# Kernel optimization log

Measured on AMD Instinct MI355X. Metric: run time of the kernel, lower is better.

The kernel has to match this reference:

```python
import jax, jax.numpy as jnp
import numpy as np

N_IN, D_IN, N_OUT, D_OUT = 1152, 8, 10, 16
ROUTINGS, NUM_BG = 3, 1
C, H, W = 1, 28, 28
BATCH = 128
DEC_IN = N_OUT * D_OUT  # 160, projection_type=None -> dec_feature_size = outcaps_size


def squash(x, axis=-1):
    norm = jnp.linalg.norm(x, axis=axis, keepdims=True)
    scale = norm ** 2 / (1.0 + norm ** 2) / (norm + 1e-8)
    return scale * x


def scale_coef(x, num_bg):
    # x: [B, n_out] or [B, n_out, n_in]; min/max normalize over dim 1,
    # excluding the last num_bg (background) capsules, then floor at 0.5.
    if num_bg > 0:
        xm = x[:, : x.shape[1] - num_bg]
    else:
        xm = x
    mn = jnp.min(xm, axis=1, keepdims=True)
    mx = jnp.max(xm, axis=1, keepdims=True)
    out = (xm - mn) / jnp.maximum(mx - mn, 1e-6)  # vrange (0,1)
    if num_bg > 0:
        out = jnp.concatenate([out, jnp.zeros_like(out[:, :num_bg])], axis=1)
    return jnp.maximum(out, 0.5)


def decode(capsflat, W1, b1, W2, b2, W3, b3):
    # fcn decoder (eval mode: dropout is identity): 160 -> 512 -> 1024 -> C*H*W
    h = jax.nn.relu(capsflat @ W1 + b1)
    h = jax.nn.relu(h @ W2 + b2)
    return jax.nn.sigmoid(h @ W3 + b3)


def setup_inputs() -> dict:
    key = jax.random.key(0)
    ks = jax.random.split(key, 9)
    return {
        'incaps': jax.random.normal(ks[0], (BATCH, N_IN, D_IN), jnp.float32),
        'x_input': jax.random.uniform(ks[1], (BATCH, C, H, W), jnp.float32),
        'weight': 0.1 * jax.random.normal(ks[2], (N_OUT, N_IN, D_OUT, D_IN), jnp.float32),
        'W1': 0.05 * jax.random.normal(ks[3], (DEC_IN, 512), jnp.float32),
        'b1': jnp.zeros((512,), jnp.float32),
        'W2': 0.05 * jax.random.normal(ks[4], (512, 1024), jnp.float32),
        'b2': jnp.zeros((1024,), jnp.float32),
        'W3': 0.05 * jax.random.normal(ks[5], (1024, C * H * W), jnp.float32),
        'b3': jnp.zeros((C * H * W,), jnp.float32),
    }


def reference(incaps, x_input, weight, W1, b1, W2, b2, W3, b3):
    B = incaps.shape[0]
    # outcaps_hat: matmul(weight, incaps[:,None,:,:,None]).squeeze(-1)
    hat = jnp.einsum('nkoi,bki->bnko', weight, incaps)  # [B, n_out, n_in, d_out]
    hat_d = jax.lax.stop_gradient(hat)
    rc = jnp.ones((B, N_OUT, N_IN), hat.dtype)
    eye = jnp.eye(N_OUT, dtype=hat.dtype)
    x_flat = x_input.reshape(B, 1, -1)
    for _ in range(ROUTINGS - 1):
        # squash over capsule dim, weighted sum over input capsules
        outcaps = squash(jnp.sum(rc[..., None] * hat_d, axis=2, keepdims=True))  # [B,n,1,d]
        b = jnp.sum(outcaps * hat_d, axis=-1)  # agreement [B, n_out, n_in]
        c = scale_coef(b, NUM_BG)
        objcaps = outcaps[:, :, 0, :]  # [B, n_out, d_out]
        # get_every_obj_rscore vectorized: mask one object capsule at a time
        masked = objcaps[:, None, :, :] * eye[None, :, :, None]  # [B, n_obj, n_out, d]
        recon = decode(masked.reshape(B, N_OUT, DEC_IN), W1, b1, W2, b2, W3, b3)  # [B,n_obj,CHW]
        rscore = -jnp.sum((x_flat - recon) ** 2, axis=-1)  # neg MSE-sum, [B, n_obj]
        r = scale_coef(rscore, NUM_BG)
        rc = c * r[:, :, None]
    # final iteration uses non-detached hat
    outcaps = squash(jnp.sum(rc[..., None] * hat, axis=2, keepdims=True))
    return outcaps[:, :, 0, :]  # [B, n_out, d_out]
```

## Files before the change

kernel.cpp:

```cpp
#include <hip/hip_runtime.h>
#include <math.h>

#define BATCH  128
#define NIN    1152
#define DIN    8
#define NOUTC  10
#define DOUT   16
#define H1DIM  512
#define H2DIM  1024
#define PIX    784
#define NROWS  (BATCH * NOUTC)
#define NBY3   13

typedef __attribute__((ext_vector_type(8))) __bf16 bf16x8;
typedef __attribute__((ext_vector_type(4))) float  f32x4;
typedef __attribute__((ext_vector_type(4))) unsigned int u32x4;

__device__ __forceinline__ float bf2f(unsigned int u) {
    union { unsigned int i; float f; } v; v.i = u << 16; return v.f;
}
__device__ __forceinline__ ushort f2bf(float f) {
    union { float f; unsigned int i; } v; v.f = f;
    unsigned int r = v.i + 0x7FFFu + ((v.i >> 16) & 1u);
    return (ushort)(r >> 16);
}
__device__ __forceinline__ float ldin(const void* p, size_t i, int isbf) {
    return isbf ? bf2f(((const ushort*)p)[i]) : ((const float*)p)[i];
}
__device__ __forceinline__ bf16x8 ld_frag(const ushort* p) {
    uint4 u = *(const uint4*)p;
    return __builtin_bit_cast(bf16x8, u);
}
__device__ __forceinline__ float dot8(uint4 a, uint4 b) {
    float s;
    s  = bf2f(a.x & 0xffffu) * bf2f(b.x & 0xffffu);
    s += bf2f(a.x >> 16)     * bf2f(b.x >> 16);
    s += bf2f(a.y & 0xffffu) * bf2f(b.y & 0xffffu);
    s += bf2f(a.y >> 16)     * bf2f(b.y >> 16);
    s += bf2f(a.z & 0xffffu) * bf2f(b.z & 0xffffu);
    s += bf2f(a.z >> 16)     * bf2f(b.z >> 16);
    s += bf2f(a.w & 0xffffu) * bf2f(b.w & 0xffffu);
    s += bf2f(a.w >> 16)     * bf2f(b.w >> 16);
    return s;
}

struct PrepArgs {
    const void* src[9];
    ushort*     dst[9];
    int         n[9];
    int*        flag;
};

__global__ __launch_bounds__(256) void prep_kernel(PrepArgs a)
{
    __shared__ int cntS;
    __shared__ ushort tile[32][33];
    int tid = threadIdx.x;
    if (tid == 0) cntS = 0;
    __syncthreads();
    {
        const ushort* wu = (const ushort*)a.src[0];
        int c = 0;
        for (int s = tid; s < 512; s += 256) {
            int e = (wu[s * 2] >> 7) & 0xFF;
            if (e >= 88 && e <= 140) c++;
        }
        atomicAdd(&cntS, c);
    }
    __syncthreads();
    int isbf = (cntS >= 384) ? 1 : 0;
    int seg = blockIdx.y;
    if (seg == 0 && blockIdx.x == 0 && tid == 0) *a.flag = isbf;

    if (seg <= 6) {
        int n = a.n[seg];
        int stride = gridDim.x * 256;
        ushort* d = a.dst[seg];
        if (isbf) {
            const ushort* s = (const ushort*)a.src[seg];
            for (int i = blockIdx.x * 256 + tid; i < n; i += stride) d[i] = s[i];
        } else {
            const float* s = (const float*)a.src[seg];
            for (int i = blockIdx.x * 256 + tid; i < n; i += stride) d[i] = f2bf(s[i]);
        }
        return;
    }
    int R = (seg == 7) ? H1DIM : H2DIM;
    int C = (seg == 7) ? H2DIM : PIX;
    int tilesX = (seg == 7) ? 32 : 25;
    int tilesY = (seg == 7) ? 16 : 32;
    int t = blockIdx.x;
    if (t >= tilesX * tilesY) return;
    int tx2 = t % tilesX, ty2 = t / tilesX;
    int c0 = tx2 * 32, r0 = ty2 * 32;
    const void* in = a.src[seg];
    ushort* out = a.dst[seg];
    int tx = tid & 31, ty = tid >> 5;
    for (int i = ty; i < 32; i += 8) {
        int r = r0 + i, c = c0 + tx;
        tile[i][tx] = (r < R && c < C) ? f2bf(ldin(in, (size_t)r * C + c, isbf)) : (ushort)0;
    }
    __syncthreads();
    for (int i = ty; i < 32; i += 8) {
        int c = c0 + i, r = r0 + tx;
        if (c < C && r < R) out[(size_t)c * R + r] = tile[tx][i];
    }
}

__global__ __launch_bounds__(256) void hat_build(
    const ushort* __restrict__ icvt,
    const ushort* __restrict__ wcvt,
    ushort* __restrict__ hatG)
{
    int kc = blockIdx.x, bc = blockIdx.y, n = blockIdx.z;
    int t  = threadIdx.x;
    int k  = kc * 128 + (t >> 1);
    int oh = (t & 1) << 3;

    const uint4* wp = (const uint4*)(wcvt + (((size_t)n * NIN + k) * DOUT + oh) * DIN);
    uint4 wr[8];
    #pragma unroll
    for (int j = 0; j < 8; j++) wr[j] = wp[j];

    int b0 = bc * 16;
    #pragma unroll 4
    for (int bl = 0; bl < 16; bl++) {
        int b = b0 + bl;
        uint4 iu = *(const uint4*)(icvt + ((size_t)b * NIN + k) * DIN);
        unsigned int h[8];
        #pragma unroll
        for (int j = 0; j < 8; j++) h[j] = f2bf(dot8(wr[j], iu));
        u32x4 ov = { h[0] | (h[1] << 16), h[2] | (h[3] << 16),
                     h[4] | (h[5] << 16), h[6] | (h[7] << 16) };
        __builtin_nontemporal_store(ov,
            (u32x4*)(hatG + (((size_t)(b * NOUTC + n) * NIN + k) * DOUT + oh)));
    }
}

template<bool COMPUTE>
__global__ __launch_bounds__(512, 8) void reduce_pass(
    const ushort* __restrict__ hatG,
    const ushort* __restrict__ icvt,
    const ushort* __restrict__ wcvt,
    const ushort* __restrict__ bsPrev,
    const float*  __restrict__ partials,
    int iter0,
    const ushort* __restrict__ W1c,
    const ushort* __restrict__ b1c,
    ushort* __restrict__ h1out,
    ushort* __restrict__ bsOut,
    void*   __restrict__ outFinal,
    const int* __restrict__ flagp)
{
    int bn  = blockIdx.x;
    int n   = bn % NOUTC;
    int b   = bn / NOUTC;
    int tid = threadIdx.x;

    __shared__ uint4  hatS4[NIN * DOUT / 8];
    __shared__ ushort wSb[NIN];
    __shared__ float  redS[8][16];
    __shared__ float  sumS[16];
    __shared__ float  ocS[16];
    __shared__ float  scaleS;
    ushort* hatS = (ushort*)hatS4;

    if constexpr (COMPUTE) {
        __shared__ uint4 incS4[NIN * DIN / 8];
        const uint4* incp = (const uint4*)(icvt + (size_t)b * NIN * DIN);
        for (int i = tid; i < NIN * DIN / 8; i += 512) incS4[i] = incp[i];
        __syncthreads();
        const ushort* incS = (const ushort*)incS4;
        const ushort* wp = wcvt + (size_t)n * NIN * DOUT * DIN;
        for (int idx = tid; idx < NIN * DOUT; idx += 512) {
            int k = idx >> 4;
            uint4 wu = *(const uint4*)(wp + (size_t)idx * 8);
            uint4 iu = *(const uint4*)(incS + k * 8);
            hatS[idx] = f2bf(dot8(wu, iu));
        }
    } else {
        const u32x4* hp = (const u32x4*)(hatG + (size_t)bn * NIN * DOUT);
        for (int i = tid; i < NIN * DOUT / 8; i += 512) {
            u32x4 v = __builtin_nontemporal_load(hp + i);
            hatS4[i] = __builtin_bit_cast(uint4, v);
        }
    }

    if (!iter0) {
        if (tid < 9) {
            float s = 0.f;
            #pragma unroll
            for (int j = 0; j < NBY3; j++)
                s += partials[(size_t)(b * NOUTC + tid) * 16 + j];
            sumS[tid] = -s;
        }
        __syncthreads();
        float mn = 1e30f, mx = -1e30f;
        #pragma unroll
        for (int n2 = 0; n2 < 9; n2++) {
            float v = sumS[n2];
            mn = fminf(mn, v); mx = fmaxf(mx, v);
        }
        float den = fmaxf(mx - mn, 1e-6f);
        float rv = (n < 9) ? fmaxf((sumS[n] - mn) / den, 0.5f) : 0.5f;
        for (int k = tid; k < NIN; k += 512) {
            float c = 0.5f;
            if (n < 9) {
                float vv[9], mn2 = 1e30f, mx2 = -1e30f;
                #pragma unroll
                for (int n2 = 0; n2 < 9; n2++) {
                    vv[n2] = bf2f(bsPrev[(size_t)(b * NOUTC + n2) * NIN + k]);
                    mn2 = fminf(mn2, vv[n2]); mx2 = fmaxf(mx2, vv[n2]);
                }
                float den2 = fmaxf(mx2 - mn2, 1e-6f);
                c = fmaxf((vv[n] - mn2) / den2, 0.5f);
            }
            wSb[k] = f2bf(c * rv);
        }
    }
    __syncthreads();

    int h = tid & 1, kb = tid >> 1;
    int wave = tid >> 6, lane = tid & 63;
    float acc[8];
    #pragma unroll
    for (int o = 0; o < 8; o++) acc[o] = 0.f;
    #pragma unroll
    for (int j = 0; j < 4; j++) {
        int k = kb + 256 * j;
        float w = iter0 ? 1.f : bf2f(wSb[k]);
        bf16x8 hv = ld_frag(hatS + k * 16 + h * 8);
        #pragma unroll
        for (int o = 0; o < 8; o++) acc[o] += w * (float)hv[o];
    }
    if (kb < 128) {
        int k = 1024 + kb;
        float w = iter0 ? 1.f : bf2f(wSb[k]);
        bf16x8 hv = ld_frag(hatS + k * 16 + h * 8);
        #pragma unroll
        for (int o = 0; o < 8; o++) acc[o] += w * (float)hv[o];
    }
    #pragma unroll
    for (int off = 32; off >= 2; off >>= 1) {
        #pragma unroll
        for (int o = 0; o < 8; o++) acc[o] += __shfl_xor(acc[o], off);
    }
    if (lane < 2) {
        #pragma unroll
        for (int o = 0; o < 8; o++) redS[wave][lane * 8 + o] = acc[o];
    }
    __syncthreads();
    if (tid < 16) {
        float s = 0.f;
        #pragma unroll
        for (int wv = 0; wv < 8; wv++) s += redS[wv][tid];
        sumS[tid] = s;
    }
    __syncthreads();
    if (tid == 0) {
        float n2 = 0.f;
        #pragma unroll
        for (int o = 0; o < 16; o++) n2 += sumS[o] * sumS[o];
        float nrm = sqrtf(n2);
        scaleS = n2 / (1.f + n2) / (nrm + 1e-8f);
    }
    __syncthreads();
    if (tid < 16) {
        float oc = scaleS * sumS[tid];
        ocS[tid] = oc;
        if (outFinal) {
            if (*flagp) ((ushort*)outFinal)[(size_t)bn * 16 + tid] = f2bf(oc);
            else        ((float*) outFinal)[(size_t)bn * 16 + tid] = oc;
        }
    }
    __syncthreads();

    if (bsOut) {
        #pragma unroll
        for (int j = 0; j < 4; j++) {
            int k = kb + 256 * j;
            bf16x8 hv = ld_frag(hatS + k * 16 + h * 8);
            float s = 0.f;
            #pragma unroll
            for (int o = 0; o < 8; o++) s += ocS[h * 8 + o] * (float)hv[o];
            s += __shfl_xor(s, 1);
            if (h == 0) bsOut[(size_t)bn * NIN + k] = f2bf(s);
        }
        if (kb < 128) {
            int k = 1024 + kb;
            bf16x8 hv = ld_frag(hatS + k * 16 + h * 8);
            float s = 0.f;
            #pragma unroll
            for (int o = 0; o < 8; o++) s += ocS[h * 8 + o] * (float)hv[o];
            s += __shfl_xor(s, 1);
            if (h == 0) bsOut[(size_t)bn * NIN + k] = f2bf(s);
        }
    }

    if (h1out) {
        int col = tid;
        float acc1 = bf2f(b1c[col]);
        #pragma unroll
        for (int i = 0; i < 16; i++)
            acc1 += ocS[i] * bf2f(W1c[(size_t)(n * 16 + i) * H1DIM + col]);
        h1out[(size_t)bn * H1DIM + col] = f2bf(fmaxf(acc1, 0.f));
    }
}

__global__ __launch_bounds__(256) void gemm_kernel(
    const ushort* __restrict__ A, const ushort* __restrict__ Bt,
    const ushort* __restrict__ bias, int K, int N,
    ushort* __restrict__ Cout,
    const ushort* __restrict__ xin, float* __restrict__ partials)
{
    int m0 = blockIdx.x * 64, n0 = blockIdx.y * 64;
    int tid = threadIdx.x;
    int wave = tid >> 6, lane = tid & 63, quad = lane >> 4, l16 = lane & 15;

    __shared__ uint4 As4[320];
    __shared__ uint4 Bs4[320];
    ushort* As = (ushort*)As4;
    ushort* Bs = (ushort*)Bs4;

    f32x4 acc[4];
    #pragma unroll
    for (int nt = 0; nt < 4; nt++)
        #pragma unroll
        for (int rg = 0; rg < 4; rg++) acc[nt][rg] = 0.f;

    int sMi = tid >> 2, sKk = (tid & 3) * 8;
    int sLds = sMi * 5 + (tid & 3);
    const ushort* Ap = A + (size_t)(m0 + sMi) * K + sKk;
    const ushort* Bp = Bt + (size_t)(n0 + sMi) * K + sKk;
    bool bOK = (n0 + sMi) < N;

    uint4 aR = *(const uint4*)Ap;
    uint4 bR = bOK ? *(const uint4*)Bp : make_uint4(0, 0, 0, 0);

    for (int k0 = 0; k0 < K; k0 += 32) {
        As4[sLds] = aR;
        Bs4[sLds] = bR;
        __syncthreads();
        if (k0 + 32 < K) {
            aR = *(const uint4*)(Ap + k0 + 32);
            bR = bOK ? *(const uint4*)(Bp + k0 + 32) : make_uint4(0, 0, 0, 0);
        }
        bf16x8 a = ld_frag(As + (wave * 16 + l16) * 40 + quad * 8);
        #pragma unroll
        for (int nt = 0; nt < 4; nt++) {
            bf16x8 bb = ld_frag(Bs + (nt * 16 + l16) * 40 + quad * 8);
            acc[nt] = __builtin_amdgcn_mfma_f32_16x16x32_bf16(a, bb, acc[nt], 0, 0, 0);
        }
        __syncthreads();
    }

    int rowBase = m0 + wave * 16 + quad * 4;
    if (Cout) {
        #pragma unroll
        for (int nt = 0; nt < 4; nt++) {
            int col = n0 + nt * 16 + l16;
            float bv = bf2f(bias[col]);
            #pragma unroll
            for (int rg = 0; rg < 4; rg++) {
                float v = acc[nt][rg] + bv;
                Cout[(size_t)(rowBase + rg) * N + col] = f2bf(fmaxf(v, 0.f));
            }
        }
    } else {
        float vr[4] = {0.f, 0.f, 0.f, 0.f};
        #pragma unroll
        for (int nt = 0; nt < 4; nt++) {
            int col = n0 + nt * 16 + l16;
            if (col < N) {
                float bv = bf2f(bias[col]);
                #pragma unroll
                for (int rg = 0; rg < 4; rg++) {
                    int row = rowBase + rg;
                    int bb = row / NOUTC;
                    float z = acc[nt][rg] + bv;
                    float s = 1.f / (1.f + __expf(-z));
                    float d = bf2f(xin[(size_t)bb * PIX + col]) - s;
                    vr[rg] += d * d;
                }
            }
        }
        #pragma unroll
        for (int rg = 0; rg < 4; rg++) {
            float v = vr[rg];
            #pragma unroll
            for (int off = 8; off >= 1; off >>= 1) v += __shfl_xor(v, off, 16);
            if (l16 == 0)
                partials[(size_t)(rowBase + rg) * 16 + blockIdx.y] = v;
        }
    }
}

extern "C" void kernel_launch(void* const* d_in, const int* in_sizes, int n_in,
                              void* d_out, int out_size, void* d_ws, size_t ws_size,
                              hipStream_t stream)
{
    const void* inc = d_in[0];
    const void* x   = d_in[1];
    const void* w   = d_in[2];
    const void* W1  = d_in[3];
    const void* b1  = d_in[4];
    const void* W2  = d_in[5];
    const void* b2  = d_in[6];
    const void* W3  = d_in[7];
    const void* b3  = d_in[8];

    char* p = (char*)d_ws;
    auto alloc = [&](size_t bytes) { void* r = p; p += (bytes + 255) & ~(size_t)255; return r; };
    int*    flagWS    = (int*)alloc(256);
    ushort* bsA       = (ushort*)alloc((size_t)NROWS * NIN * 2);
    ushort* bsB       = (ushort*)alloc((size_t)NROWS * NIN * 2);
    float*  partials  = (float*)alloc((size_t)NROWS * 16 * 4);
    ushort* h1WS      = (ushort*)alloc((size_t)NROWS * H1DIM * 2);
    ushort* h2WS      = (ushort*)alloc((size_t)NROWS * H2DIM * 2);
    ushort* W2T       = (ushort*)alloc((size_t)H2DIM * H1DIM * 2);
    ushort* W3T       = (ushort*)alloc((size_t)PIX * H2DIM * 2);
    ushort* wcvt      = (ushort*)alloc((size_t)NOUTC * NIN * DOUT * DIN * 2);
    ushort* icvt      = (ushort*)alloc((size_t)BATCH * NIN * DIN * 2);
    ushort* W1c       = (ushort*)alloc((size_t)160 * H1DIM * 2);
    ushort* b1c       = (ushort*)alloc((size_t)H1DIM * 2);
    ushort* b2c       = (ushort*)alloc((size_t)H2DIM * 2);
    ushort* b3c       = (ushort*)alloc((size_t)PIX * 2);
    ushort* xc        = (ushort*)alloc((size_t)BATCH * PIX * 2);
    ushort* hatG      = (ushort*)alloc((size_t)NROWS * NIN * DOUT * 2);
    bool haveHat = ((char*)hatG + (size_t)NROWS * NIN * DOUT * 2) <= ((char*)d_ws + ws_size);

    PrepArgs pa;
    pa.src[0] = w;   pa.dst[0] = wcvt; pa.n[0] = NOUTC * NIN * DOUT * DIN;
    pa.src[1] = inc; pa.dst[1] = icvt; pa.n[1] = BATCH * NIN * DIN;
    pa.src[2] = W1;  pa.dst[2] = W1c;  pa.n[2] = 160 * H1DIM;
    pa.src[3] = b1;  pa.dst[3] = b1c;  pa.n[3] = H1DIM;
    pa.src[4] = b2;  pa.dst[4] = b2c;  pa.n[4] = H2DIM;
    pa.src[5] = b3;  pa.dst[5] = b3c;  pa.n[5] = PIX;
    pa.src[6] = x;   pa.dst[6] = xc;   pa.n[6] = BATCH * PIX;
    pa.src[7] = W2;  pa.dst[7] = W2T;  pa.n[7] = 0;
    pa.src[8] = W3;  pa.dst[8] = W3T;  pa.n[8] = 0;
    pa.flag = flagWS;
    prep_kernel<<<dim3(800, 9), 256, 0, stream>>>(pa);

    if (haveHat) hat_build<<<dim3(9, 8, NOUTC), 256, 0, stream>>>(icvt, wcvt, hatG);

    if (haveHat)
        reduce_pass<false><<<NROWS, 512, 0, stream>>>(
            hatG, icvt, wcvt, nullptr, nullptr, 1,
            W1c, b1c, h1WS, bsA, nullptr, flagWS);
    else
        reduce_pass<true><<<NROWS, 512, 0, stream>>>(
            nullptr, icvt, wcvt, nullptr, nullptr, 1,
            W1c, b1c, h1WS, bsA, nullptr, flagWS);

    for (int it = 0; it < 2; it++) {
        gemm_kernel<<<dim3(NROWS / 64, H2DIM / 64), 256, 0, stream>>>(
            h1WS, W2T, b2c, H1DIM, H2DIM, h2WS, nullptr, nullptr);
        gemm_kernel<<<dim3(NROWS / 64, NBY3), 256, 0, stream>>>(
            h2WS, W3T, b3c, H2DIM, PIX, nullptr, xc, partials);

        int last = (it == 1);
        const ushort* bsP = (it == 0) ? bsA : bsB;
        ushort* bsO       = last ? nullptr : bsB;
        ushort* h1o       = last ? nullptr : h1WS;
        void*   fin       = last ? d_out : nullptr;
        if (haveHat)
            reduce_pass<false><<<NROWS, 512, 0, stream>>>(
                hatG, icvt, wcvt, bsP, partials, 0,
                W1c, b1c, h1o, bsO, fin, flagWS);
        else
            reduce_pass<true><<<NROWS, 512, 0, stream>>>(
                nullptr, icvt, wcvt, bsP, partials, 0,
                W1c, b1c, h1o, bsO, fin, flagWS);
    }
}
```

Baseline: 215.3 us.

## Read raw inputs in hat_build and keep hat fragments in registers in reduce_pass

Drops the separate bf16 conversion of the capsule weight and input tensors from the prep kernel. hat_build and the compute fallback now read the raw inputs directly and convert them on the fly, after detecting the input dtype. In the main reduce_pass path, each thread keeps its hat fragments in registers instead of staging the whole 36 KB hat tile through shared memory, and only the tail rows go to shared memory. This cuts the LDS footprint and shared-memory traffic, and the occupancy hint is lowered to 4 to make room for the extra register pressure.

```diff
diff --git a/kernel.cpp b/kernel.cpp
--- a/kernel.cpp
+++ b/kernel.cpp
@@ -27,9 +27,11 @@
 __device__ __forceinline__ float ldin(const void* p, size_t i, int isbf) {
     return isbf ? bf2f(((const ushort*)p)[i]) : ((const float*)p)[i];
 }
+__device__ __forceinline__ bf16x8 frag_of(uint4 u) {
+    return __builtin_bit_cast(bf16x8, u);
+}
 __device__ __forceinline__ bf16x8 ld_frag(const ushort* p) {
-    uint4 u = *(const uint4*)p;
-    return __builtin_bit_cast(bf16x8, u);
+    return frag_of(*(const uint4*)p);
 }
 __device__ __forceinline__ float dot8(uint4 a, uint4 b) {
     float s;
@@ -43,11 +45,35 @@
     s += bf2f(a.w >> 16)     * bf2f(b.w >> 16);
     return s;
 }
+__device__ __forceinline__ uint4 pack8(float4 a, float4 b) {
+    uint4 r;
+    r.x = f2bf(a.x) | ((unsigned)f2bf(a.y) << 16);
+    r.y = f2bf(a.z) | ((unsigned)f2bf(a.w) << 16);
+    r.z = f2bf(b.x) | ((unsigned)f2bf(b.y) << 16);
+    r.w = f2bf(b.z) | ((unsigned)f2bf(b.w) << 16);
+    return r;
+}
+
+__device__ __forceinline__ int detect_bf(const void* w, int* cntS) {
+    int tid = threadIdx.x, nt = blockDim.x;
+    if (tid == 0) *cntS = 0;
+    __syncthreads();
+    const ushort* u = (const ushort*)w;
+    int c = 0;
+    for (int s = tid; s < 512; s += nt) {
+        int e = (u[s * 2] >> 7) & 0xFF;
+        if (e >= 88 && e <= 140) c++;
+    }
+    atomicAdd(cntS, c);
+    __syncthreads();
+    return (*cntS >= 384) ? 1 : 0;
+}
 
 struct PrepArgs {
-    const void* src[9];
-    ushort*     dst[9];
-    int         n[9];
+    const void* w;
+    const void* src[7];
+    ushort*     dst[7];
+    int         n[7];
     int*        flag;
 };
 
@@ -56,23 +82,11 @@
     __shared__ int cntS;
     __shared__ ushort tile[32][33];
     int tid = threadIdx.x;
-    if (tid == 0) cntS = 0;
-    __syncthreads();
-    {
-        const ushort* wu = (const ushort*)a.src[0];
-        int c = 0;
-        for (int s = tid; s < 512; s += 256) {
-            int e = (wu[s * 2] >> 7) & 0xFF;
-            if (e >= 88 && e <= 140) c++;
-        }
-        atomicAdd(&cntS, c);
-    }
-    __syncthreads();
-    int isbf = (cntS >= 384) ? 1 : 0;
+    int isbf = detect_bf(a.w, &cntS);
     int seg = blockIdx.y;
     if (seg == 0 && blockIdx.x == 0 && tid == 0) *a.flag = isbf;
 
-    if (seg <= 6) {
+    if (seg <= 4) {
         int n = a.n[seg];
         int stride = gridDim.x * 256;
         ushort* d = a.dst[seg];
@@ -85,10 +99,10 @@
         }
         return;
     }
-    int R = (seg == 7) ? H1DIM : H2DIM;
-    int C = (seg == 7) ? H2DIM : PIX;
-    int tilesX = (seg == 7) ? 32 : 25;
-    int tilesY = (seg == 7) ? 16 : 32;
+    int R = (seg == 5) ? H1DIM : H2DIM;
+    int C = (seg == 5) ? H2DIM : PIX;
+    int tilesX = (seg == 5) ? 32 : 25;
+    int tilesY = (seg == 5) ? 16 : 32;
     int t = blockIdx.x;
     if (t >= tilesX * tilesY) return;
     int tx2 = t % tilesX, ty2 = t / tilesX;
@@ -108,25 +122,40 @@
 }
 
 __global__ __launch_bounds__(256) void hat_build(
-    const ushort* __restrict__ icvt,
-    const ushort* __restrict__ wcvt,
+    const void* __restrict__ inc,
+    const void* __restrict__ w,
     ushort* __restrict__ hatG)
 {
+    __shared__ int cntS;
+    int isbf = detect_bf(w, &cntS);
     int kc = blockIdx.x, bc = blockIdx.y, n = blockIdx.z;
     int t  = threadIdx.x;
     int k  = kc * 128 + (t >> 1);
     int oh = (t & 1) << 3;
 
-    const uint4* wp = (const uint4*)(wcvt + (((size_t)n * NIN + k) * DOUT + oh) * DIN);
+    size_t wbase = ((size_t)n * NIN + k) * DOUT + oh;
     uint4 wr[8];
-    #pragma unroll
-    for (int j = 0; j < 8; j++) wr[j] = wp[j];
+    if (isbf) {
+        const uint4* wp = (const uint4*)((const ushort*)w + wbase * DIN);
+        #pragma unroll
+        for (int j = 0; j < 8; j++) wr[j] = wp[j];
+    } else {
+        const float4* wp = (const float4*)((const float*)w + wbase * DIN);
+        #pragma unroll
+        for (int j = 0; j < 8; j++) wr[j] = pack8(wp[2 * j], wp[2 * j + 1]);
+    }
 
     int b0 = bc * 16;
     #pragma unroll 4
     for (int bl = 0; bl < 16; bl++) {
         int b = b0 + bl;
-        uint4 iu = *(const uint4*)(icvt + ((size_t)b * NIN + k) * DIN);
+        size_t ioff = ((size_t)b * NIN + k) * DIN;
+        uint4 iu;
+        if (isbf) iu = *(const uint4*)((const ushort*)inc + ioff);
+        else {
+            const float4* ip = (const float4*)((const float*)inc + ioff);
+            iu = pack8(ip[0], ip[1]);
+        }
         unsigned int h[8];
         #pragma unroll
         for (int j = 0; j < 8; j++) h[j] = f2bf(dot8(wr[j], iu));
@@ -138,10 +167,10 @@
 }
 
 template<bool COMPUTE>
-__global__ __launch_bounds__(512, 8) void reduce_pass(
+__global__ __launch_bounds__(512, 4) void reduce_pass(
     const ushort* __restrict__ hatG,
-    const ushort* __restrict__ icvt,
-    const ushort* __restrict__ wcvt,
+    const void*   __restrict__ incRaw,
+    const void*   __restrict__ wRaw,
     const ushort* __restrict__ bsPrev,
     const float*  __restrict__ partials,
     int iter0,
@@ -157,33 +186,47 @@
     int b   = bn / NOUTC;
     int tid = threadIdx.x;
 
-    __shared__ uint4  hatS4[NIN * DOUT / 8];
     __shared__ ushort wSb[NIN];
     __shared__ float  redS[8][16];
     __shared__ float  sumS[16];
     __shared__ float  ocS[16];
     __shared__ float  scaleS;
-    ushort* hatS = (ushort*)hatS4;
-
-    if constexpr (COMPUTE) {
-        __shared__ uint4 incS4[NIN * DIN / 8];
-        const uint4* incp = (const uint4*)(icvt + (size_t)b * NIN * DIN);
-        for (int i = tid; i < NIN * DIN / 8; i += 512) incS4[i] = incp[i];
-        __syncthreads();
-        const ushort* incS = (const ushort*)incS4;
-        const ushort* wp = wcvt + (size_t)n * NIN * DOUT * DIN;
+
+    int h = tid & 1, kb = tid >> 1;
+    int wave = tid >> 6, lane = tid & 63;
+
+    uint4 v[4];
+    const ushort* tailS;
+
+    if constexpr (!COMPUTE) {
+        __shared__ uint4 hatTail4[256];
+        const ushort* hbase = hatG + (size_t)bn * NIN * DOUT;
+        #pragma unroll
+        for (int j = 0; j < 4; j++)
+            v[j] = *(const uint4*)(hbase + ((kb + 256 * j) * DOUT + h * 8));
+        if (tid < 256)
+            hatTail4[tid] = *(const uint4*)(hbase + 1024 * DOUT + tid * 8);
+        tailS = (const ushort*)hatTail4;
+    } else {
+        __shared__ int cntS;
+        __shared__ uint4 hatS4[NIN * DOUT / 8];
+        int isbf = detect_bf(wRaw, &cntS);
+        size_t wnb = (size_t)n * NIN * DOUT * DIN;
         for (int idx = tid; idx < NIN * DOUT; idx += 512) {
             int k = idx >> 4;
-            uint4 wu = *(const uint4*)(wp + (size_t)idx * 8);
-            uint4 iu = *(const uint4*)(incS + k * 8);
-            hatS[idx] = f2bf(dot8(wu, iu));
-        }
-    } else {
-        const u32x4* hp = (const u32x4*)(hatG + (size_t)bn * NIN * DOUT);
-        for (int i = tid; i < NIN * DOUT / 8; i += 512) {
-            u32x4 v = __builtin_nontemporal_load(hp + i);
-            hatS4[i] = __builtin_bit_cast(uint4, v);
-        }
+            float s = 0.f;
+            #pragma unroll
+            for (int i = 0; i < 8; i++)
+                s += ldin(wRaw, wnb + (size_t)idx * 8 + i, isbf) *
+                     ldin(incRaw, ((size_t)b * NIN + k) * DIN + i, isbf);
+            ((ushort*)hatS4)[idx] = f2bf(s);
+        }
+        __syncthreads();
+        const ushort* hbase = (const ushort*)hatS4;
+        #pragma unroll
+        for (int j = 0; j < 4; j++)
+            v[j] = *(const uint4*)(hbase + ((kb + 256 * j) * DOUT + h * 8));
+        tailS = hbase + 1024 * DOUT;
     }
 
     if (!iter0) {
@@ -198,8 +241,8 @@
         float mn = 1e30f, mx = -1e30f;
         #pragma unroll
         for (int n2 = 0; n2 < 9; n2++) {
-            float v = sumS[n2];
-            mn = fminf(mn, v); mx = fmaxf(mx, v);
+            float vv = sumS[n2];
+            mn = fminf(mn, vv); mx = fmaxf(mx, vv);
         }
         float den = fmaxf(mx - mn, 1e-6f);
         float rv = (n < 9) ? fmaxf((sumS[n] - mn) / den, 0.5f) : 0.5f;
@@ -220,8 +263,6 @@
     }
     __syncthreads();
 
-    int h = tid & 1, kb = tid >> 1;
-    int wave = tid >> 6, lane = tid & 63;
     float acc[8];
     #pragma unroll
     for (int o = 0; o < 8; o++) acc[o] = 0.f;
@@ -229,14 +270,14 @@
     for (int j = 0; j < 4; j++) {
         int k = kb + 256 * j;
         float w = iter0 ? 1.f : bf2f(wSb[k]);
-        bf16x8 hv = ld_frag(hatS + k * 16 + h * 8);
+        bf16x8 hv = frag_of(v[j]);
         #pragma unroll
         for (int o = 0; o < 8; o++) acc[o] += w * (float)hv[o];
     }
-    if (kb < 128) {
+    if (tid < 256) {
         int k = 1024 + kb;
         float w = iter0 ? 1.f : bf2f(wSb[k]);
-        bf16x8 hv = ld_frag(hatS + k * 16 + h * 8);
+        bf16x8 hv = ld_frag(tailS + kb * DOUT + h * 8);
         #pragma unroll
         for (int o = 0; o < 8; o++) acc[o] += w * (float)hv[o];
     }
@@ -276,24 +317,25 @@
     __syncthreads();
 
     if (bsOut) {
+        float o0 = ocS[h * 8 + 0], o1 = ocS[h * 8 + 1], o2 = ocS[h * 8 + 2],
+              o3 = ocS[h * 8 + 3], o4 = ocS[h * 8 + 4], o5 = ocS[h * 8 + 5],
+              o6 = ocS[h * 8 + 6], o7 = ocS[h * 8 + 7];
         #pragma unroll
         for (int j = 0; j < 4; j++) {
-            int k = kb + 256 * j;
-            bf16x8 hv = ld_frag(hatS + k * 16 + h * 8);
-            float s = 0.f;
-            #pragma unroll
-            for (int o = 0; o < 8; o++) s += ocS[h * 8 + o] * (float)hv[o];
+            bf16x8 hv = frag_of(v[j]);
+            float s = o0 * (float)hv[0] + o1 * (float)hv[1] + o2 * (float)hv[2] +
+                      o3 * (float)hv[3] + o4 * (float)hv[4] + o5 * (float)hv[5] +
+                      o6 * (float)hv[6] + o7 * (float)hv[7];
             s += __shfl_xor(s, 1);
-            if (h == 0) bsOut[(size_t)bn * NIN + k] = f2bf(s);
-        }
-        if (kb < 128) {
-            int k = 1024 + kb;
-            bf16x8 hv = ld_frag(hatS + k * 16 + h * 8);
-            float s = 0.f;
-            #pragma unroll
-            for (int o = 0; o < 8; o++) s += ocS[h * 8 + o] * (float)hv[o];
+            if (h == 0) bsOut[(size_t)bn * NIN + kb + 256 * j] = f2bf(s);
+        }
+        if (tid < 256) {
+            bf16x8 hv = ld_frag(tailS + kb * DOUT + h * 8);
+            float s = o0 * (float)hv[0] + o1 * (float)hv[1] + o2 * (float)hv[2] +
+                      o3 * (float)hv[3] + o4 * (float)hv[4] + o5 * (float)hv[5] +
+                      o6 * (float)hv[6] + o7 * (float)hv[7];
             s += __shfl_xor(s, 1);
-            if (h == 0) bsOut[(size_t)bn * NIN + k] = f2bf(s);
+            if (h == 0) bsOut[(size_t)bn * NIN + 1024 + kb] = f2bf(s);
         }
     }
 
@@ -419,8 +461,6 @@
     ushort* h2WS      = (ushort*)alloc((size_t)NROWS * H2DIM * 2);
     ushort* W2T       = (ushort*)alloc((size_t)H2DIM * H1DIM * 2);
     ushort* W3T       = (ushort*)alloc((size_t)PIX * H2DIM * 2);
-    ushort* wcvt      = (ushort*)alloc((size_t)NOUTC * NIN * DOUT * DIN * 2);
-    ushort* icvt      = (ushort*)alloc((size_t)BATCH * NIN * DIN * 2);
     ushort* W1c       = (ushort*)alloc((size_t)160 * H1DIM * 2);
     ushort* b1c       = (ushort*)alloc((size_t)H1DIM * 2);
     ushort* b2c       = (ushort*)alloc((size_t)H2DIM * 2);
@@ -430,27 +470,26 @@
     bool haveHat = ((char*)hatG + (size_t)NROWS * NIN * DOUT * 2) <= ((char*)d_ws + ws_size);
 
     PrepArgs pa;
-    pa.src[0] = w;   pa.dst[0] = wcvt; pa.n[0] = NOUTC * NIN * DOUT * DIN;
-    pa.src[1] = inc; pa.dst[1] = icvt; pa.n[1] = BATCH * NIN * DIN;
-    pa.src[2] = W1;  pa.dst[2] = W1c;  pa.n[2] = 160 * H1DIM;
-    pa.src[3] = b1;  pa.dst[3] = b1c;  pa.n[3] = H1DIM;
-    pa.src[4] = b2;  pa.dst[4] = b2c;  pa.n[4] = H2DIM;
-    pa.src[5] = b3;  pa.dst[5] = b3c;  pa.n[5] = PIX;
-    pa.src[6] = x;   pa.dst[6] = xc;   pa.n[6] = BATCH * PIX;
-    pa.src[7] = W2;  pa.dst[7] = W2T;  pa.n[7] = 0;
-    pa.src[8] = W3;  pa.dst[8] = W3T;  pa.n[8] = 0;
+    pa.w = w;
+    pa.src[0] = W1;  pa.dst[0] = W1c;  pa.n[0] = 160 * H1DIM;
+    pa.src[1] = b1;  pa.dst[1] = b1c;  pa.n[1] = H1DIM;
+    pa.src[2] = b2;  pa.dst[2] = b2c;  pa.n[2] = H2DIM;
+    pa.src[3] = b3;  pa.dst[3] = b3c;  pa.n[3] = PIX;
+    pa.src[4] = x;   pa.dst[4] = xc;   pa.n[4] = BATCH * PIX;
+    pa.src[5] = W2;  pa.dst[5] = W2T;  pa.n[5] = 0;
+    pa.src[6] = W3;  pa.dst[6] = W3T;  pa.n[6] = 0;
     pa.flag = flagWS;
-    prep_kernel<<<dim3(800, 9), 256, 0, stream>>>(pa);
-
-    if (haveHat) hat_build<<<dim3(9, 8, NOUTC), 256, 0, stream>>>(icvt, wcvt, hatG);
+    prep_kernel<<<dim3(800, 7), 256, 0, stream>>>(pa);
+
+    if (haveHat) hat_build<<<dim3(9, 8, NOUTC), 256, 0, stream>>>(inc, w, hatG);
 
     if (haveHat)
         reduce_pass<false><<<NROWS, 512, 0, stream>>>(
-            hatG, icvt, wcvt, nullptr, nullptr, 1,
+            hatG, inc, w, nullptr, nullptr, 1,
             W1c, b1c, h1WS, bsA, nullptr, flagWS);
     else
         reduce_pass<true><<<NROWS, 512, 0, stream>>>(
-            nullptr, icvt, wcvt, nullptr, nullptr, 1,
+            nullptr, inc, w, nullptr, nullptr, 1,
             W1c, b1c, h1WS, bsA, nullptr, flagWS);
 
     for (int it = 0; it < 2; it++) {
@@ -466,11 +505,11 @@
         void*   fin       = last ? d_out : nullptr;
         if (haveHat)
             reduce_pass<false><<<NROWS, 512, 0, stream>>>(
-                hatG, icvt, wcvt, bsP, partials, 0,
+                hatG, inc, w, bsP, partials, 0,
                 W1c, b1c, h1o, bsO, fin, flagWS);
         else
             reduce_pass<true><<<NROWS, 512, 0, stream>>>(
-                nullptr, icvt, wcvt, bsP, partials, 0,
+                nullptr, inc, w, bsP, partials, 0,
                 W1c, b1c, h1o, bsO, fin, flagWS);
     }
 }
```

New measurement: 213.2 us. About the same (-1.0%).
